# Performance work log

Hardware: AMD Instinct MI355X
Metric: run time of the kernel (lower is better)

Reference implementation:

```python
import jax, jax.numpy as jnp
import numpy as np

TAU = 0.1  # temperature (registered buffer, non-trainable)
EPS = 1e-12  # F.normalize eps


def setup_inputs() -> dict:
    key = jax.random.key(0)
    k1, k2 = jax.random.split(key)
    B, C = 4096, 512
    z1 = jax.random.normal(k1, (B, C), dtype=jnp.float32)
    z2 = jax.random.normal(k2, (B, C), dtype=jnp.float32)
    return {"z1": z1, "z2": z2}


def _l2_normalize(x):
    # matches F.normalize(p=2, dim=1): x / max(||x||, eps)
    n = jnp.sqrt(jnp.sum(x * x, axis=1, keepdims=True))
    return x / jnp.maximum(n, EPS)


def reference(z1, z2):
    B = z1.shape[0]
    N = 2 * B
    z = jnp.concatenate([_l2_normalize(z1), _l2_normalize(z2)], axis=0)  # [2B, C]
    # cosine similarity of unit vectors == dot product -> single GEMM
    S = jnp.exp((z @ z.T) / TAU)  # [2B, 2B]
    rows = jnp.arange(N)
    pos_cols = (rows + B) % N  # mask[r, c]=1 iff r == (c+B) mod 2B  <=> c == (r+B) mod 2B
    positive = S[rows, pos_cols]                 # [2B]
    # negatives = row sum over ~mask; note the original INCLUDES the diagonal
    negative = jnp.sum(S, axis=1) - positive     # [2B]
    pairs_loss = -jnp.log(positive / negative)   # [2B]
    loss = pairs_loss.reshape(2, B).sum(axis=0) / N  # [B]
    return loss.mean()  # reduce=True
```

## Files before the change

### kernel.cpp

```cpp
#include <hip/hip_runtime.h>
#include <hip/hip_bf16.h>


#define BDIM 4096
#define CDIM 512
#define NROWS 8192
#define NTILE 32
#define NBLK 528

typedef __attribute__((ext_vector_type(4))) float f32x4;
typedef __attribute__((ext_vector_type(8))) short bf16x8;

__device__ __forceinline__ unsigned short f2bf_rne(float x) {
    unsigned u = __float_as_uint(x);
    u += 0x7fffu + ((u >> 16) & 1u);
    return (unsigned short)(u >> 16);
}

__global__ __launch_bounds__(256) void normalize_kernel(
    const float* __restrict__ z1, const float* __restrict__ z2,
    unsigned short* __restrict__ zb, float* __restrict__ pos10,
    float* __restrict__ rowsum, float* __restrict__ out) {
    if (blockIdx.x == 0) {
#pragma unroll
        for (int i = 0; i < NROWS / 256; ++i) rowsum[i * 256 + threadIdx.x] = 0.f;
        if (threadIdx.x == 0) out[0] = 0.f;
    }
    const int w = threadIdx.x >> 6, lane = threadIdx.x & 63;
    const int r = blockIdx.x * 4 + w;
    const float4* p1 = (const float4*)(z1 + (size_t)r * CDIM);
    const float4* p2 = (const float4*)(z2 + (size_t)r * CDIM);
    float4 a0 = p1[lane], a1 = p1[64 + lane];
    float4 b0 = p2[lane], b1 = p2[64 + lane];
    float s1 = a0.x * a0.x + a0.y * a0.y + a0.z * a0.z + a0.w * a0.w +
               a1.x * a1.x + a1.y * a1.y + a1.z * a1.z + a1.w * a1.w;
    float s2 = b0.x * b0.x + b0.y * b0.y + b0.z * b0.z + b0.w * b0.w +
               b1.x * b1.x + b1.y * b1.y + b1.z * b1.z + b1.w * b1.w;
    float d = a0.x * b0.x + a0.y * b0.y + a0.z * b0.z + a0.w * b0.w +
              a1.x * b1.x + a1.y * b1.y + a1.z * b1.z + a1.w * b1.w;
#pragma unroll
    for (int m = 1; m < 64; m <<= 1) {
        s1 += __shfl_xor(s1, m, 64);
        s2 += __shfl_xor(s2, m, 64);
        d += __shfl_xor(d, m, 64);
    }
    const float n1 = fmaxf(sqrtf(s1), 1e-12f);
    const float n2 = fmaxf(sqrtf(s2), 1e-12f);
    const float i1 = 1.0f / n1, i2 = 1.0f / n2;
    ushort4 o;
    ushort4* q1 = (ushort4*)(zb + (size_t)r * CDIM);
    ushort4* q2 = (ushort4*)(zb + (size_t)(r + BDIM) * CDIM);
    o.x = f2bf_rne(a0.x * i1); o.y = f2bf_rne(a0.y * i1);
    o.z = f2bf_rne(a0.z * i1); o.w = f2bf_rne(a0.w * i1);
    q1[lane] = o;
    o.x = f2bf_rne(a1.x * i1); o.y = f2bf_rne(a1.y * i1);
    o.z = f2bf_rne(a1.z * i1); o.w = f2bf_rne(a1.w * i1);
    q1[64 + lane] = o;
    o.x = f2bf_rne(b0.x * i2); o.y = f2bf_rne(b0.y * i2);
    o.z = f2bf_rne(b0.z * i2); o.w = f2bf_rne(b0.w * i2);
    q2[lane] = o;
    o.x = f2bf_rne(b1.x * i2); o.y = f2bf_rne(b1.y * i2);
    o.z = f2bf_rne(b1.z * i2); o.w = f2bf_rne(b1.w * i2);
    q2[64 + lane] = o;
    if (lane == 0) pos10[r] = (d / (n1 * n2)) * 10.0f;
}

__global__ __launch_bounds__(512, 2) void simgemm_kernel(
    const unsigned short* __restrict__ Z, float* __restrict__ rowsum) {
    int by = 0, rem = blockIdx.x;
    while (rem >= NTILE - by) { rem -= NTILE - by; ++by; }
    const int bx = by + rem;
    const bool diag = (bx == by);

    __shared__ unsigned short lds[2][2][256 * 64];

    const int t = threadIdx.x;
    const int lane = t & 63, w = t >> 6;
    const int wr = w >> 2, wc = w & 3;

    f32x4 acc[8][4] = {};

    const int srow = t >> 3;
    const int scolb = (((t & 7) ^ ((t >> 3) & 7)) << 4);
    const char* Zb = (const char*)Z;
    const size_t apan = ((size_t)(by * 256) << 10);
    const size_t bpan = ((size_t)(bx * 256) << 10);

#define STAGE(kt, db)                                                             \
    {                                                                             \
        const int kb_ = ((kt) << 7) + scolb;                                      \
        _Pragma("unroll") for (int i_ = 0; i_ < 4; ++i_) {                        \
            const size_t ro_ = ((size_t)(i_ * 64 + srow) << 10) + kb_;            \
            __builtin_amdgcn_global_load_lds(                                     \
                (const __attribute__((address_space(1))) void*)(Zb + apan + ro_), \
                (__attribute__((address_space(3))) void*)((char*)&lds[db][0][0] + i_ * 8192 + w * 1024), \
                16, 0, 0);                                                        \
            __builtin_amdgcn_global_load_lds(                                     \
                (const __attribute__((address_space(1))) void*)(Zb + bpan + ro_), \
                (__attribute__((address_space(3))) void*)((char*)&lds[db][1][0] + i_ * 8192 + w * 1024), \
                16, 0, 0);                                                        \
        }                                                                         \
    }

    STAGE(0, 0);
    asm volatile("s_waitcnt vmcnt(0)\n\ts_barrier" ::: "memory");

    const int swz = (lane & 7) << 4;
#pragma unroll
    for (int it = 0; it < 8; ++it) {
        const int cur = it & 1;
        if (it < 7) {
            STAGE(it + 1, cur ^ 1);
            asm volatile("s_waitcnt vmcnt(8)\n\ts_barrier" ::: "memory");
        } else {
            asm volatile("s_waitcnt vmcnt(0)\n\ts_barrier" ::: "memory");
        }

        const char* Ab = (const char*)&lds[cur][0][0];
        const char* Bb = (const char*)&lds[cur][1][0];
#pragma unroll
        for (int kk = 0; kk < 2; ++kk) {
            const int koff = (kk * 64 + ((lane >> 4) << 4)) ^ swz;
            bf16x8 af[8], bfr[4];
#pragma unroll
            for (int mi = 0; mi < 8; ++mi) {
                const int row = wr * 128 + mi * 16 + (lane & 15);
                af[mi] = *(const bf16x8*)(Ab + row * 128 + koff);
            }
#pragma unroll
            for (int ni = 0; ni < 4; ++ni) {
                const int row = wc * 64 + ni * 16 + (lane & 15);
                bfr[ni] = *(const bf16x8*)(Bb + row * 128 + koff);
            }
#pragma unroll
            for (int mi = 0; mi < 8; ++mi)
#pragma unroll
                for (int ni = 0; ni < 4; ++ni)
                    acc[mi][ni] = __builtin_amdgcn_mfma_f32_16x16x32_bf16(
                        af[mi], bfr[ni], acc[mi][ni], 0, 0, 0);
        }
        asm volatile("s_barrier" ::: "memory");
    }
#undef STAGE

    const float SC = 14.4269504088896340736f;
    const int g = lane >> 4;
    float cs[4] = {0.f, 0.f, 0.f, 0.f};
#pragma unroll
    for (int mi = 0; mi < 8; ++mi) {
        float rs0 = 0.f, rs1 = 0.f, rs2 = 0.f, rs3 = 0.f;
#pragma unroll
        for (int ni = 0; ni < 4; ++ni) {
            f32x4 a = acc[mi][ni];
            const float e0 = exp2f(a[0] * SC);
            const float e1 = exp2f(a[1] * SC);
            const float e2 = exp2f(a[2] * SC);
            const float e3 = exp2f(a[3] * SC);
            rs0 += e0; rs1 += e1; rs2 += e2; rs3 += e3;
            cs[ni] += (e0 + e1) + (e2 + e3);
        }
#pragma unroll
        for (int m = 1; m < 16; m <<= 1) {
            rs0 += __shfl_xor(rs0, m, 64);
            rs1 += __shfl_xor(rs1, m, 64);
            rs2 += __shfl_xor(rs2, m, 64);
            rs3 += __shfl_xor(rs3, m, 64);
        }
        if ((lane & 15) == 0) {
            const int rbase = by * 256 + wr * 128 + mi * 16 + g * 4;
            atomicAdd(&rowsum[rbase + 0], rs0);
            atomicAdd(&rowsum[rbase + 1], rs1);
            atomicAdd(&rowsum[rbase + 2], rs2);
            atomicAdd(&rowsum[rbase + 3], rs3);
        }
    }
    if (!diag) {
#pragma unroll
        for (int ni = 0; ni < 4; ++ni) {
            float c = cs[ni];
            c += __shfl_xor(c, 16, 64);
            c += __shfl_xor(c, 32, 64);
            if (lane < 16)
                atomicAdd(&rowsum[bx * 256 + wc * 64 + ni * 16 + lane], c);
        }
    }
}

__global__ __launch_bounds__(256) void finalize_kernel(
    const float* __restrict__ rowsum, const float* __restrict__ pos10,
    float* __restrict__ out) {
    __shared__ float sm[4];
    const int w = threadIdx.x >> 6, lane = threadIdx.x & 63;
    const int r = blockIdx.x * 256 + threadIdx.x;
    const float p10 = pos10[r];
    const float pos = expf(p10);
    float l = (logf(rowsum[r] - pos) - p10) +
              (logf(rowsum[r + BDIM] - pos) - p10);
#pragma unroll
    for (int m = 1; m < 64; m <<= 1) l += __shfl_xor(l, m, 64);
    if (lane == 0) sm[w] = l;
    __syncthreads();
    if (threadIdx.x == 0) {
        const float tot = sm[0] + sm[1] + sm[2] + sm[3];
        atomicAdd(out, tot * (1.0f / ((float)NROWS * (float)BDIM)));
    }
}

extern "C" void kernel_launch(void* const* d_in, const int* in_sizes, int n_in,
                              void* d_out, int out_size, void* d_ws, size_t ws_size,
                              hipStream_t stream) {
    const float* z1 = (const float*)d_in[0];
    const float* z2 = (const float*)d_in[1];
    float* out = (float*)d_out;
    unsigned short* zb = (unsigned short*)d_ws;
    float* rowsum = (float*)((char*)d_ws + (size_t)NROWS * CDIM * 2);
    float* pos10 = rowsum + NROWS;

    normalize_kernel<<<BDIM / 4, 256, 0, stream>>>(z1, z2, zb, pos10, rowsum, out);
    simgemm_kernel<<<NBLK, 512, 0, stream>>>(zb, rowsum);
    finalize_kernel<<<BDIM / 256, 256, 0, stream>>>(rowsum, pos10, out);
}
```

Measured before the change: 142.0 us.

## Split GEMM K-loop into four quadrant phases with interleaved async LDS loads

Restructures the similarity GEMM main loop into four sub-phases, each computing one quadrant of the per-wave output tile. Global-to-LDS loads for the next K-tile are issued in quarter-panel chunks between the phases. The LDS layout is split into four 128-row panels, and s_setprio is raised around the MFMA bursts. The aim is finer-grained overlap of memory traffic with matrix math and fewer fragment registers live at once, at the cost of many more barriers per iteration.

```diff
diff --git a/kernel.cpp b/kernel.cpp
--- a/kernel.cpp
+++ b/kernel.cpp
@@ -7,9 +7,13 @@
 #define NROWS 8192
 #define NTILE 32
 #define NBLK 528
+#define NKT 8
 
 typedef __attribute__((ext_vector_type(4))) float f32x4;
 typedef __attribute__((ext_vector_type(8))) short bf16x8;
+
+#define AS1 __attribute__((address_space(1)))
+#define AS3 __attribute__((address_space(3)))
 
 __device__ __forceinline__ unsigned short f2bf_rne(float x) {
     unsigned u = __float_as_uint(x);
@@ -72,7 +76,7 @@
     const int bx = by + rem;
     const bool diag = (bx == by);
 
-    __shared__ unsigned short lds[2][2][256 * 64];
+    __shared__ unsigned short lds[2][4][128 * 64];
 
     const int t = threadIdx.x;
     const int lane = t & 63, w = t >> 6;
@@ -86,62 +90,121 @@
     const size_t apan = ((size_t)(by * 256) << 10);
     const size_t bpan = ((size_t)(bx * 256) << 10);
 
-#define STAGE(kt, db)                                                             \
-    {                                                                             \
-        const int kb_ = ((kt) << 7) + scolb;                                      \
-        _Pragma("unroll") for (int i_ = 0; i_ < 4; ++i_) {                        \
-            const size_t ro_ = ((size_t)(i_ * 64 + srow) << 10) + kb_;            \
-            __builtin_amdgcn_global_load_lds(                                     \
-                (const __attribute__((address_space(1))) void*)(Zb + apan + ro_), \
-                (__attribute__((address_space(3))) void*)((char*)&lds[db][0][0] + i_ * 8192 + w * 1024), \
-                16, 0, 0);                                                        \
-            __builtin_amdgcn_global_load_lds(                                     \
-                (const __attribute__((address_space(1))) void*)(Zb + bpan + ro_), \
-                (__attribute__((address_space(3))) void*)((char*)&lds[db][1][0] + i_ * 8192 + w * 1024), \
-                16, 0, 0);                                                        \
-        }                                                                         \
-    }
-
-    STAGE(0, 0);
-    asm volatile("s_waitcnt vmcnt(0)\n\ts_barrier" ::: "memory");
-
+#define STG(T, J)                                                                \
+    {                                                                            \
+        const size_t pb_ = ((J) < 2 ? apan : bpan);                              \
+        const char* g0_ = Zb + pb_ +                                             \
+            ((size_t)((((J) & 1) * 128) + srow) << 10) + ((T) * 128) + scolb;    \
+        char* d0_ = (char*)&lds[(T) & 1][J][0] + w * 1024;                       \
+        __builtin_amdgcn_global_load_lds((const AS1 void*)g0_,                   \
+                                         (AS3 void*)d0_, 16, 0, 0);              \
+        __builtin_amdgcn_global_load_lds((const AS1 void*)(g0_ + (64 << 10)),    \
+                                         (AS3 void*)(d0_ + 8192), 16, 0, 0);     \
+    }
+
+    STG(0, 2); STG(0, 3); STG(0, 0); STG(0, 1); STG(1, 2); STG(1, 0);
+    asm volatile("s_waitcnt vmcnt(4)\n\ts_barrier" ::: "memory");
+
+    const int arow = lane & 15;
+    const int brow0 = (wc & 1) * 64;
+    const int klo = (lane >> 4) << 4;
     const int swz = (lane & 7) << 4;
-#pragma unroll
-    for (int it = 0; it < 8; ++it) {
-        const int cur = it & 1;
-        if (it < 7) {
-            STAGE(it + 1, cur ^ 1);
-            asm volatile("s_waitcnt vmcnt(8)\n\ts_barrier" ::: "memory");
-        } else {
-            asm volatile("s_waitcnt vmcnt(0)\n\ts_barrier" ::: "memory");
-        }
-
-        const char* Ab = (const char*)&lds[cur][0][0];
-        const char* Bb = (const char*)&lds[cur][1][0];
-#pragma unroll
-        for (int kk = 0; kk < 2; ++kk) {
-            const int koff = (kk * 64 + ((lane >> 4) << 4)) ^ swz;
-            bf16x8 af[8], bfr[4];
-#pragma unroll
-            for (int mi = 0; mi < 8; ++mi) {
-                const int row = wr * 128 + mi * 16 + (lane & 15);
-                af[mi] = *(const bf16x8*)(Ab + row * 128 + koff);
-            }
-#pragma unroll
-            for (int ni = 0; ni < 4; ++ni) {
-                const int row = wc * 64 + ni * 16 + (lane & 15);
-                bfr[ni] = *(const bf16x8*)(Bb + row * 128 + koff);
-            }
-#pragma unroll
-            for (int mi = 0; mi < 8; ++mi)
-#pragma unroll
-                for (int ni = 0; ni < 4; ++ni)
+
+#pragma unroll
+    for (int T = 0; T < NKT; ++T) {
+        const int buf = T & 1;
+        const char* Ab = (const char*)&lds[buf][wr][0];
+        const char* Bb = (const char*)&lds[buf][2 + (wc >> 1)][0];
+        if (T >= 1) {
+            if (T < NKT - 1)
+                asm volatile("s_waitcnt vmcnt(4)\n\ts_barrier" ::: "memory");
+            else
+                asm volatile("s_waitcnt vmcnt(0)\n\ts_barrier" ::: "memory");
+        }
+
+        bf16x8 af[4][2], bf[4][2];
+
+#pragma unroll
+        for (int mi = 0; mi < 4; ++mi)
+#pragma unroll
+            for (int kk = 0; kk < 2; ++kk)
+                af[mi][kk] = *(const bf16x8*)(Ab + (mi * 16 + arow) * 128 +
+                                              ((kk * 64 + klo) ^ swz));
+#pragma unroll
+        for (int ni = 0; ni < 2; ++ni)
+#pragma unroll
+            for (int kk = 0; kk < 2; ++kk)
+                bf[ni][kk] = *(const bf16x8*)(Bb + (brow0 + ni * 16 + arow) * 128 +
+                                              ((kk * 64 + klo) ^ swz));
+        if (T + 1 < NKT) STG(T + 1, 3);
+        asm volatile("s_barrier" ::: "memory");
+        __builtin_amdgcn_s_setprio(1);
+#pragma unroll
+        for (int mi = 0; mi < 4; ++mi)
+#pragma unroll
+            for (int ni = 0; ni < 2; ++ni)
+#pragma unroll
+                for (int kk = 0; kk < 2; ++kk)
                     acc[mi][ni] = __builtin_amdgcn_mfma_f32_16x16x32_bf16(
-                        af[mi], bfr[ni], acc[mi][ni], 0, 0, 0);
-        }
-        asm volatile("s_barrier" ::: "memory");
-    }
-#undef STAGE
+                        af[mi][kk], bf[ni][kk], acc[mi][ni], 0, 0, 0);
+        __builtin_amdgcn_s_setprio(0);
+        asm volatile("s_waitcnt lgkmcnt(0)\n\ts_barrier" ::: "memory");
+
+#pragma unroll
+        for (int ni = 2; ni < 4; ++ni)
+#pragma unroll
+            for (int kk = 0; kk < 2; ++kk)
+                bf[ni][kk] = *(const bf16x8*)(Bb + (brow0 + ni * 16 + arow) * 128 +
+                                              ((kk * 64 + klo) ^ swz));
+        if (T + 1 < NKT) STG(T + 1, 1);
+        asm volatile("s_barrier" ::: "memory");
+        __builtin_amdgcn_s_setprio(1);
+#pragma unroll
+        for (int mi = 0; mi < 4; ++mi)
+#pragma unroll
+            for (int ni = 2; ni < 4; ++ni)
+#pragma unroll
+                for (int kk = 0; kk < 2; ++kk)
+                    acc[mi][ni] = __builtin_amdgcn_mfma_f32_16x16x32_bf16(
+                        af[mi][kk], bf[ni][kk], acc[mi][ni], 0, 0, 0);
+        __builtin_amdgcn_s_setprio(0);
+        asm volatile("s_waitcnt lgkmcnt(0)\n\ts_barrier" ::: "memory");
+
+#pragma unroll
+        for (int mi = 0; mi < 4; ++mi)
+#pragma unroll
+            for (int kk = 0; kk < 2; ++kk)
+                af[mi][kk] = *(const bf16x8*)(Ab + ((mi + 4) * 16 + arow) * 128 +
+                                              ((kk * 64 + klo) ^ swz));
+        if (T + 2 < NKT) STG(T + 2, 2);
+        asm volatile("s_barrier" ::: "memory");
+        __builtin_amdgcn_s_setprio(1);
+#pragma unroll
+        for (int mi = 0; mi < 4; ++mi)
+#pragma unroll
+            for (int ni = 0; ni < 2; ++ni)
+#pragma unroll
+                for (int kk = 0; kk < 2; ++kk)
+                    acc[mi + 4][ni] = __builtin_amdgcn_mfma_f32_16x16x32_bf16(
+                        af[mi][kk], bf[ni][kk], acc[mi + 4][ni], 0, 0, 0);
+        __builtin_amdgcn_s_setprio(0);
+        asm volatile("s_waitcnt lgkmcnt(0)\n\ts_barrier" ::: "memory");
+
+        if (T + 2 < NKT) STG(T + 2, 0);
+        asm volatile("s_barrier" ::: "memory");
+        __builtin_amdgcn_s_setprio(1);
+#pragma unroll
+        for (int mi = 0; mi < 4; ++mi)
+#pragma unroll
+            for (int ni = 2; ni < 4; ++ni)
+#pragma unroll
+                for (int kk = 0; kk < 2; ++kk)
+                    acc[mi + 4][ni] = __builtin_amdgcn_mfma_f32_16x16x32_bf16(
+                        af[mi][kk], bf[ni][kk], acc[mi + 4][ni], 0, 0, 0);
+        __builtin_amdgcn_s_setprio(0);
+        asm volatile("s_waitcnt lgkmcnt(0)\n\ts_barrier" ::: "memory");
+    }
+#undef STG
 
     const float SC = 14.4269504088896340736f;
     const int g = lane >> 4;
```

After: 143.3 us. About the same (+0.9%).
